# Optimization experiments

Hardware: AMD Instinct MI355X
Metric: run time of the kernel (lower is better)

The kernel has to match this reference:

```python
import jax, jax.numpy as jnp
import numpy as np

HIDDEN = 2048
NUM_HEADS = 32
NUM_GROUPS = 8
HEAD_DIM = HIDDEN // NUM_HEADS          # 64
GROUP_DIM = HEAD_DIM * NUM_GROUPS       # 512
HPG = NUM_HEADS // NUM_GROUPS           # heads per group = 4
B, S = 2, 2048


def setup_inputs() -> dict:
    key = jax.random.key(0)
    ks = jax.random.split(key, 6)
    sd = 1.0 / np.sqrt(HIDDEN)
    return {
        "x": jax.random.normal(ks[0], (B, S, HIDDEN), jnp.float32),
        "mask": jnp.ones((1, 1, S, S), jnp.int32),
        "Wq": jax.random.normal(ks[1], (HIDDEN, HIDDEN), jnp.float32) * sd,
        "bq": jnp.zeros((HIDDEN,), jnp.float32),
        "Wk": jax.random.normal(ks[2], (HIDDEN, GROUP_DIM), jnp.float32) * sd,
        "bk": jnp.zeros((GROUP_DIM,), jnp.float32),
        "Wv": jax.random.normal(ks[3], (HIDDEN, GROUP_DIM), jnp.float32) * sd,
        "bv": jnp.zeros((GROUP_DIM,), jnp.float32),
        "Wo": jax.random.normal(ks[4], (HIDDEN, HIDDEN), jnp.float32) * sd,
        "bo": jnp.zeros((HIDDEN,), jnp.float32),
    }


def reference(x, mask, Wq, bq, Wk, bk, Wv, bv, Wo, bo):
    b, s, _ = x.shape
    # projections
    q = x @ Wq + bq                                        # [B,S,H*d]
    k = x @ Wk + bk                                        # [B,S,G*d]
    v = x @ Wv + bv
    # split heads: q heads are group-major (g, p) to match the torch view
    q = q.reshape(b, s, NUM_GROUPS, HPG, HEAD_DIM)         # [B,S,G,P,d]
    k = k.reshape(b, s, NUM_GROUPS, HEAD_DIM)              # [B,S,G,d]
    v = v.reshape(b, s, NUM_GROUPS, HEAD_DIM)
    scale = 1.0 / np.sqrt(HEAD_DIM).astype(np.float32)
    # grouped attention without materializing repeated K/V
    scores = jnp.einsum('bsgpd,btgd->bgpst', q, k) * scale  # [B,G,P,S,T]
    if mask is not None:
        m = mask[:, :, None]                                # [1,1,1,S,T]
        scores = jnp.where(m == 0, jnp.float32(-1e9), scores)
    weights = jax.nn.softmax(scores, axis=-1)
    out = jnp.einsum('bgpst,btgd->bsgpd', weights, v)       # [B,S,G,P,d]
    out = out.reshape(b, s, HIDDEN)
    return out @ Wo + bo
```

## Files before the change

### kernel.cpp

```cpp
#include <hip/hip_runtime.h>
#include <hip/hip_bf16.h>


#define DEVINL __device__ __forceinline__

typedef __attribute__((ext_vector_type(8))) short bf16x8;
typedef __attribute__((ext_vector_type(4))) float f32x4;

DEVINL unsigned short f2bf(float f) {
  unsigned u = __builtin_bit_cast(unsigned, f);
  u += 0x7fffu + ((u >> 16) & 1u);
  return (unsigned short)(u >> 16);
}

DEVINL unsigned pk2bf(float a, float b) {
  __hip_bfloat162 h = __float22bfloat162_rn(float2{a, b});
  unsigned r;
  __builtin_memcpy(&r, &h, 4);
  return r;
}

DEVINL void gl_lds16(const void* g, void* l) {
  __builtin_amdgcn_global_load_lds(
      (const __attribute__((address_space(1))) void*)g,
      (__attribute__((address_space(3))) void*)l, 16, 0, 0);
}

__global__ __launch_bounds__(256)
void prep_k(const float* __restrict__ x,
            const float* __restrict__ Wq, const float* __restrict__ Wk,
            const float* __restrict__ Wv, const float* __restrict__ Wo,
            const int* __restrict__ mask,
            unsigned short* __restrict__ xb,
            unsigned short* __restrict__ WqT, unsigned short* __restrict__ WkT,
            unsigned short* __restrict__ WvT, unsigned short* __restrict__ WoT,
            int* __restrict__ flags)
{
  __shared__ float tile[64][68];
  __shared__ int fl[4];
  int blk = blockIdx.x;
  const int tid = threadIdx.x;
  if (blk < 4096) {
    size_t base = (size_t)blk * 2048 + tid * 8;
    float4 f0 = *(const float4*)&x[base];
    float4 f1 = *(const float4*)&x[base + 4];
    uint4 o;
    o.x = pk2bf(f0.x, f0.y); o.y = pk2bf(f0.z, f0.w);
    o.z = pk2bf(f1.x, f1.y); o.w = pk2bf(f1.z, f1.w);
    *(uint4*)&xb[base] = o;
    return;
  }
  blk -= 4096;
  if (blk >= 2560) {
    int fb = blk - 2560;
    int qt = fb >> 5, tt = fb & 31;
    bool hz = false;
#pragma unroll
    for (int it = 0; it < 8; ++it) {
      int l = it * 1024 + tid * 4;
      int row = l >> 6, col = l & 63;
      int4 mv = *(const int4*)&mask[(size_t)(qt * 128 + row) * 2048 + tt * 64 + col];
      hz |= (mv.x == 0) | (mv.y == 0) | (mv.z == 0) | (mv.w == 0);
    }
    unsigned long long bal = __ballot(hz);
    if ((tid & 63) == 0) fl[tid >> 6] = (bal != 0ull) ? 1 : 0;
    __syncthreads();
    if (tid == 0) flags[fb] = fl[0] | fl[1] | fl[2] | fl[3];
    return;
  }
  const float* W; unsigned short* WT; int N;
  if (blk < 1024)      { W = Wq; WT = WqT; N = 2048; }
  else if (blk < 1280) { W = Wk; WT = WkT; N = 512;  blk -= 1024; }
  else if (blk < 1536) { W = Wv; WT = WvT; N = 512;  blk -= 1280; }
  else                 { W = Wo; WT = WoT; N = 2048; blk -= 1536; }
  const int kt = blk & 31, nt = blk >> 5;
  const int k0 = kt * 64, n0 = nt * 64;
  const int tr = tid >> 4, tc4 = (tid & 15) * 4;
#pragma unroll
  for (int it = 0; it < 4; ++it) {
    int k = it * 16 + tr;
    float4 v = *(const float4*)&W[(size_t)(k0 + k) * N + n0 + tc4];
    tile[tc4 + 0][k] = v.x; tile[tc4 + 1][k] = v.y;
    tile[tc4 + 2][k] = v.z; tile[tc4 + 3][k] = v.w;
  }
  __syncthreads();
#pragma unroll
  for (int it = 0; it < 4; ++it) {
    int n = it * 16 + tr;
    uint2 o;
    o.x = pk2bf(tile[n][tc4 + 0], tile[n][tc4 + 1]);
    o.y = pk2bf(tile[n][tc4 + 2], tile[n][tc4 + 3]);
    *(uint2*)&WT[(size_t)(n0 + n) * 2048 + k0 + tc4] = o;
  }
}

__global__ __launch_bounds__(256)
void mm_qkv(const unsigned short* __restrict__ A,
            const unsigned short* __restrict__ Wt,
            const float* __restrict__ bq, const float* __restrict__ bk,
            const float* __restrict__ bv,
            unsigned short* __restrict__ qb, unsigned short* __restrict__ kb,
            unsigned short* __restrict__ vb)
{
  __shared__ __align__(16) unsigned short As[128 * 32];
  __shared__ __align__(16) unsigned short Bs[128 * 32];
  const int tid = threadIdx.x;
  const int lane = tid & 63, w = tid >> 6;
  const int l15 = lane & 15, quad = lane >> 4;
  const int wm = w & 1, wn = w >> 1;
  const int row0 = blockIdx.y * 128;
  const int col0 = blockIdx.x * 128;

  f32x4 acc[4][4];
#pragma unroll
  for (int mt = 0; mt < 4; ++mt)
#pragma unroll
    for (int nt = 0; nt < 4; ++nt) acc[mt][nt] = (f32x4){0.f, 0.f, 0.f, 0.f};

  const int c0 = tid, c1 = 256 + tid;
  const size_t aoff0 = (size_t)(row0 + (c0 >> 2)) * 2048 + (c0 & 3) * 8;
  const size_t aoff1 = (size_t)(row0 + (c1 >> 2)) * 2048 + (c1 & 3) * 8;
  const size_t boff0 = (size_t)(col0 + (c0 >> 2)) * 2048 + (c0 & 3) * 8;
  const size_t boff1 = (size_t)(col0 + (c1 >> 2)) * 2048 + (c1 & 3) * 8;

  for (int k0 = 0; k0 < 2048; k0 += 32) {
    gl_lds16(A + aoff0 + k0, As + (size_t)c0 * 8);
    gl_lds16(A + aoff1 + k0, As + (size_t)c1 * 8);
    gl_lds16(Wt + boff0 + k0, Bs + (size_t)c0 * 8);
    gl_lds16(Wt + boff1 + k0, Bs + (size_t)c1 * 8);
    __syncthreads();
    bf16x8 af[4], bfr[4];
#pragma unroll
    for (int mt = 0; mt < 4; ++mt)
      af[mt] = *(const bf16x8*)&As[(wm * 64 + mt * 16 + l15) * 32 + quad * 8];
#pragma unroll
    for (int nt = 0; nt < 4; ++nt)
      bfr[nt] = *(const bf16x8*)&Bs[(wn * 64 + nt * 16 + l15) * 32 + quad * 8];
#pragma unroll
    for (int mt = 0; mt < 4; ++mt)
#pragma unroll
      for (int nt = 0; nt < 4; ++nt)
        acc[mt][nt] = __builtin_amdgcn_mfma_f32_16x16x32_bf16(
            af[mt], bfr[nt], acc[mt][nt], 0, 0, 0);
    __syncthreads();
  }

  const int rbase = row0 + wm * 64 + quad * 4;
#pragma unroll
  for (int nt = 0; nt < 4; ++nt) {
    const int cg = col0 + wn * 64 + nt * 16 + l15;
#pragma unroll
    for (int mt = 0; mt < 4; ++mt) {
#pragma unroll
      for (int reg = 0; reg < 4; ++reg) {
        const int r = rbase + mt * 16 + reg;
        const int bb = r >> 11, ss = r & 2047;
        float v = acc[mt][nt][reg];
        if (col0 < 2048) {
          v += bq[cg];
          int g = cg >> 8, p = (cg >> 6) & 3, d = cg & 63;
          qb[(((size_t)((bb * 8 + g) * 4 + p)) * 2048 + ss) * 64 + d] =
              f2bf(v * 0.1803368801111244f);
        } else if (col0 < 2560) {
          int cl = cg - 2048;
          v += bk[cl];
          int g = cl >> 6, d = cl & 63;
          kb[((size_t)(bb * 8 + g) * 2048 + ss) * 64 + d] = f2bf(v);
        } else {
          int cl = cg - 2560;
          v += bv[cl];
          int g = cl >> 6, d = cl & 63;
          vb[((size_t)(bb * 8 + g) * 64 + d) * 2048 + ss] = f2bf(v);
        }
      }
    }
  }
}

__global__ __launch_bounds__(256)
void mm_out(const unsigned short* __restrict__ A,
            const unsigned short* __restrict__ Bt,
            const float* __restrict__ bias, float* __restrict__ Of)
{
  __shared__ __align__(16) unsigned short As[128 * 32];
  __shared__ __align__(16) unsigned short Bs[128 * 32];
  const int tid = threadIdx.x;
  const int lane = tid & 63, w = tid >> 6;
  const int l15 = lane & 15, quad = lane >> 4;
  const int wm = w & 1, wn = w >> 1;
  const int row0 = blockIdx.y * 128;
  const int col0 = blockIdx.x * 128;

  f32x4 acc[4][4];
#pragma unroll
  for (int mt = 0; mt < 4; ++mt)
#pragma unroll
    for (int nt = 0; nt < 4; ++nt) acc[mt][nt] = (f32x4){0.f, 0.f, 0.f, 0.f};

  const int c0 = tid, c1 = 256 + tid;
  const size_t aoff0 = (size_t)(row0 + (c0 >> 2)) * 2048 + (c0 & 3) * 8;
  const size_t aoff1 = (size_t)(row0 + (c1 >> 2)) * 2048 + (c1 & 3) * 8;
  const size_t boff0 = (size_t)(col0 + (c0 >> 2)) * 2048 + (c0 & 3) * 8;
  const size_t boff1 = (size_t)(col0 + (c1 >> 2)) * 2048 + (c1 & 3) * 8;

  for (int k0 = 0; k0 < 2048; k0 += 32) {
    gl_lds16(A + aoff0 + k0, As + (size_t)c0 * 8);
    gl_lds16(A + aoff1 + k0, As + (size_t)c1 * 8);
    gl_lds16(Bt + boff0 + k0, Bs + (size_t)c0 * 8);
    gl_lds16(Bt + boff1 + k0, Bs + (size_t)c1 * 8);
    __syncthreads();
    bf16x8 af[4], bfr[4];
#pragma unroll
    for (int mt = 0; mt < 4; ++mt)
      af[mt] = *(const bf16x8*)&As[(wm * 64 + mt * 16 + l15) * 32 + quad * 8];
#pragma unroll
    for (int nt = 0; nt < 4; ++nt)
      bfr[nt] = *(const bf16x8*)&Bs[(wn * 64 + nt * 16 + l15) * 32 + quad * 8];
#pragma unroll
    for (int mt = 0; mt < 4; ++mt)
#pragma unroll
      for (int nt = 0; nt < 4; ++nt)
        acc[mt][nt] = __builtin_amdgcn_mfma_f32_16x16x32_bf16(
            af[mt], bfr[nt], acc[mt][nt], 0, 0, 0);
    __syncthreads();
  }

  const int rbase = row0 + wm * 64 + quad * 4;
#pragma unroll
  for (int nt = 0; nt < 4; ++nt) {
    const int cg = col0 + wn * 64 + nt * 16 + l15;
    const float bvv = bias[cg];
#pragma unroll
    for (int mt = 0; mt < 4; ++mt)
#pragma unroll
      for (int reg = 0; reg < 4; ++reg) {
        const int r = rbase + mt * 16 + reg;
        Of[(size_t)r * 2048 + cg] = acc[mt][nt][reg] + bvv;
      }
  }
}

__global__ __launch_bounds__(256, 4)
void attn_k(const unsigned short* __restrict__ qb,
            const unsigned short* __restrict__ kb,
            const unsigned short* __restrict__ vb,
            const int* __restrict__ mask, const int* __restrict__ flags,
            unsigned short* __restrict__ attnb)
{
  __shared__ __align__(16) unsigned short Ks[64 * 64];
  __shared__ __align__(16) unsigned short Vs[64 * 64];
  __shared__ __align__(16) unsigned short Ps[128 * 72];
  const int tid = threadIdx.x;
  const int lane = tid & 63, w = tid >> 6;
  const int l15 = lane & 15, quad = lane >> 4;
  const int q0 = blockIdx.x * 128;
  const int pr = blockIdx.y;
  const int b = pr >> 5, g = (pr >> 2) & 7, p = pr & 3;
  const int bg = b * 8 + g;

  const unsigned short* Kg = kb + (size_t)bg * 2048 * 64;
  const unsigned short* Vg = vb + (size_t)bg * 64 * 2048;
  const unsigned short* Qg = qb + (size_t)(bg * 4 + p) * 2048 * 64;

  bf16x8 qf[2][2];
#pragma unroll
  for (int u = 0; u < 2; ++u) {
    const size_t qrow = (size_t)(q0 + w * 32 + u * 16 + l15) * 64;
    qf[u][0] = *(const bf16x8*)&Qg[qrow + quad * 8];
    qf[u][1] = *(const bf16x8*)&Qg[qrow + 32 + quad * 8];
  }

  bf16x8 ones;
#pragma unroll
  for (int i = 0; i < 8; ++i) ones[i] = (short)0x3F80;

  f32x4 acc_o[4][2];
  f32x4 acc_l[2];
#pragma unroll
  for (int u = 0; u < 2; ++u) acc_l[u] = (f32x4){0.f, 0.f, 0.f, 0.f};
#pragma unroll
  for (int dt = 0; dt < 4; ++dt)
#pragma unroll
    for (int u = 0; u < 2; ++u) acc_o[dt][u] = (f32x4){0.f, 0.f, 0.f, 0.f};

  const int c0 = tid, c1 = 256 + tid;
  const int kr0 = c0 >> 3, kx0 = ((c0 & 7) ^ (kr0 & 7)) * 8;
  const int kr1 = c1 >> 3, kx1 = ((c1 & 7) ^ (kr1 & 7)) * 8;

  for (int t0 = 0; t0 < 2048; t0 += 64) {
    __syncthreads();
    gl_lds16(Kg + (size_t)(t0 + kr0) * 64 + kx0, Ks + (size_t)c0 * 8);
    gl_lds16(Kg + (size_t)(t0 + kr1) * 64 + kx1, Ks + (size_t)c1 * 8);
    gl_lds16(Vg + (size_t)kr0 * 2048 + t0 + kx0, Vs + (size_t)c0 * 8);
    gl_lds16(Vg + (size_t)kr1 * 2048 + t0 + kx1, Vs + (size_t)c1 * 8);
    __syncthreads();

    bf16x8 kf[4][2];
#pragma unroll
    for (int nt = 0; nt < 4; ++nt) {
      const int trow = nt * 16 + l15, ks = trow & 7;
      kf[nt][0] = *(const bf16x8*)&Ks[trow * 64 + ((quad ^ ks) * 8)];
      kf[nt][1] = *(const bf16x8*)&Ks[trow * 64 + (((4 + quad) ^ ks) * 8)];
    }
    const bool msk = flags[blockIdx.x * 32 + (t0 >> 6)] != 0;

#pragma unroll
    for (int u = 0; u < 2; ++u) {
      f32x4 st[4];
#pragma unroll
      for (int nt = 0; nt < 4; ++nt) {
        f32x4 z = (f32x4){0.f, 0.f, 0.f, 0.f};
        z = __builtin_amdgcn_mfma_f32_16x16x32_bf16(kf[nt][0], qf[u][0], z, 0, 0, 0);
        st[nt] = __builtin_amdgcn_mfma_f32_16x16x32_bf16(kf[nt][1], qf[u][1], z, 0, 0, 0);
      }
      if (msk) {
        const size_t mrow = (size_t)(q0 + w * 32 + u * 16 + l15) * 2048;
#pragma unroll
        for (int nt = 0; nt < 4; ++nt) {
          int4 mv = *(const int4*)&mask[mrow + t0 + nt * 16 + quad * 4];
          if (mv.x == 0) st[nt][0] = -1e30f;
          if (mv.y == 0) st[nt][1] = -1e30f;
          if (mv.z == 0) st[nt][2] = -1e30f;
          if (mv.w == 0) st[nt][3] = -1e30f;
        }
      }
      const int srow = w * 32 + u * 16 + l15;
#pragma unroll
      for (int nt = 0; nt < 4; ++nt) {
        float p0 = __builtin_amdgcn_exp2f(st[nt][0]);
        float p1 = __builtin_amdgcn_exp2f(st[nt][1]);
        float p2 = __builtin_amdgcn_exp2f(st[nt][2]);
        float p3 = __builtin_amdgcn_exp2f(st[nt][3]);
        uint2 pkd;
        pkd.x = pk2bf(p0, p1);
        pkd.y = pk2bf(p2, p3);
        *(uint2*)&Ps[srow * 72 + nt * 16 + quad * 4] = pkd;
      }
    }
    asm volatile("s_waitcnt lgkmcnt(0)" ::: "memory");

    bf16x8 pf[2][2];
#pragma unroll
    for (int u = 0; u < 2; ++u) {
      const int srow = w * 32 + u * 16 + l15;
      pf[u][0] = *(const bf16x8*)&Ps[srow * 72 + quad * 8];
      pf[u][1] = *(const bf16x8*)&Ps[srow * 72 + 32 + quad * 8];
      acc_l[u] = __builtin_amdgcn_mfma_f32_16x16x32_bf16(ones, pf[u][0], acc_l[u], 0, 0, 0);
      acc_l[u] = __builtin_amdgcn_mfma_f32_16x16x32_bf16(ones, pf[u][1], acc_l[u], 0, 0, 0);
    }
#pragma unroll
    for (int dt = 0; dt < 4; ++dt) {
      const int drow = dt * 16 + l15, ks = drow & 7;
      bf16x8 v0 = *(const bf16x8*)&Vs[drow * 64 + ((quad ^ ks) * 8)];
      bf16x8 v1 = *(const bf16x8*)&Vs[drow * 64 + (((4 + quad) ^ ks) * 8)];
#pragma unroll
      for (int u = 0; u < 2; ++u) {
        acc_o[dt][u] = __builtin_amdgcn_mfma_f32_16x16x32_bf16(v0, pf[u][0], acc_o[dt][u], 0, 0, 0);
        acc_o[dt][u] = __builtin_amdgcn_mfma_f32_16x16x32_bf16(v1, pf[u][1], acc_o[dt][u], 0, 0, 0);
      }
    }
  }

  const int hh = g * 4 + p;
#pragma unroll
  for (int u = 0; u < 2; ++u) {
    const float inv = 1.0f / acc_l[u][0];
    const int s = q0 + w * 32 + u * 16 + l15;
#pragma unroll
    for (int dt = 0; dt < 4; ++dt) {
      uint2 o;
      o.x = pk2bf(acc_o[dt][u][0] * inv, acc_o[dt][u][1] * inv);
      o.y = pk2bf(acc_o[dt][u][2] * inv, acc_o[dt][u][3] * inv);
      *(uint2*)&attnb[((size_t)(b * 2048 + s)) * 2048 + hh * 64 + dt * 16 + quad * 4] = o;
    }
  }
}

extern "C" void kernel_launch(void* const* d_in, const int* in_sizes, int n_in,
                              void* d_out, int out_size, void* d_ws, size_t ws_size,
                              hipStream_t stream)
{
  (void)in_sizes; (void)n_in; (void)out_size; (void)ws_size;
  const float* x  = (const float*)d_in[0];
  const int* mask = (const int*)d_in[1];
  const float* Wq = (const float*)d_in[2];
  const float* bq = (const float*)d_in[3];
  const float* Wk = (const float*)d_in[4];
  const float* bk = (const float*)d_in[5];
  const float* Wv = (const float*)d_in[6];
  const float* bv = (const float*)d_in[7];
  const float* Wo = (const float*)d_in[8];
  const float* bo = (const float*)d_in[9];
  float* out = (float*)d_out;

  unsigned short* xb  = (unsigned short*)d_ws;
  unsigned short* WqT = xb  + 8388608;
  unsigned short* WkT = WqT + 4194304;
  unsigned short* WvT = WkT + 1048576;
  unsigned short* WoT = WvT + 1048576;
  unsigned short* qb  = WoT + 4194304;
  unsigned short* kb  = qb  + 8388608;
  unsigned short* vb  = kb  + 2097152;
  int* flags = (int*)(vb + 2097152);
  unsigned short* attnb = xb;

  dim3 blk(256);
  hipLaunchKernelGGL(prep_k, dim3(7168), blk, 0, stream,
                     x, Wq, Wk, Wv, Wo, mask, xb, WqT, WkT, WvT, WoT, flags);
  hipLaunchKernelGGL(mm_qkv, dim3(24, 32), blk, 0, stream,
                     xb, WqT, bq, bk, bv, qb, kb, vb);
  hipLaunchKernelGGL(attn_k, dim3(16, 64), blk, 0, stream,
                     qb, kb, vb, mask, flags, attnb);
  hipLaunchKernelGGL(mm_out, dim3(16, 32), blk, 0, stream,
                     attnb, WoT, bo, out);
}
```

Before: 361.7 us.

## Double-buffer K/V tiles in attention kernel to overlap loads with compute

The attention kernel gets two shared-memory buffers each for K and V. The next 64-key tile is fetched with direct global-to-LDS loads while the current tile is processed, and each iteration now ends with a single barrier instead of two. The aim is to hide global-load latency behind the MFMA and softmax work. The cost is more LDS per block, so launch bounds drop from 4 to 3 blocks per CU, which lowers occupancy.

```diff
diff --git a/kernel.cpp b/kernel.cpp
--- a/kernel.cpp
+++ b/kernel.cpp
@@ -240,15 +240,15 @@
   }
 }
 
-__global__ __launch_bounds__(256, 4)
+__global__ __launch_bounds__(256, 3)
 void attn_k(const unsigned short* __restrict__ qb,
             const unsigned short* __restrict__ kb,
             const unsigned short* __restrict__ vb,
             const int* __restrict__ mask, const int* __restrict__ flags,
             unsigned short* __restrict__ attnb)
 {
-  __shared__ __align__(16) unsigned short Ks[64 * 64];
-  __shared__ __align__(16) unsigned short Vs[64 * 64];
+  __shared__ __align__(16) unsigned short Ks[2][64 * 64];
+  __shared__ __align__(16) unsigned short Vs[2][64 * 64];
   __shared__ __align__(16) unsigned short Ps[128 * 72];
   const int tid = threadIdx.x;
   const int lane = tid & 63, w = tid >> 6;
@@ -287,22 +287,33 @@
   const int kr0 = c0 >> 3, kx0 = ((c0 & 7) ^ (kr0 & 7)) * 8;
   const int kr1 = c1 >> 3, kx1 = ((c1 & 7) ^ (kr1 & 7)) * 8;
 
-  for (int t0 = 0; t0 < 2048; t0 += 64) {
-    __syncthreads();
-    gl_lds16(Kg + (size_t)(t0 + kr0) * 64 + kx0, Ks + (size_t)c0 * 8);
-    gl_lds16(Kg + (size_t)(t0 + kr1) * 64 + kx1, Ks + (size_t)c1 * 8);
-    gl_lds16(Vg + (size_t)kr0 * 2048 + t0 + kx0, Vs + (size_t)c0 * 8);
-    gl_lds16(Vg + (size_t)kr1 * 2048 + t0 + kx1, Vs + (size_t)c1 * 8);
-    __syncthreads();
+  gl_lds16(Kg + (size_t)kr0 * 64 + kx0, &Ks[0][(size_t)c0 * 8]);
+  gl_lds16(Kg + (size_t)kr1 * 64 + kx1, &Ks[0][(size_t)c1 * 8]);
+  gl_lds16(Vg + (size_t)kr0 * 2048 + kx0, &Vs[0][(size_t)c0 * 8]);
+  gl_lds16(Vg + (size_t)kr1 * 2048 + kx1, &Vs[0][(size_t)c1 * 8]);
+  __syncthreads();
+
+  for (int it = 0; it < 32; ++it) {
+    const int cur = it & 1;
+    const int t0 = it << 6;
+    if (it < 31) {
+      const int tn = t0 + 64;
+      gl_lds16(Kg + (size_t)(tn + kr0) * 64 + kx0, &Ks[cur ^ 1][(size_t)c0 * 8]);
+      gl_lds16(Kg + (size_t)(tn + kr1) * 64 + kx1, &Ks[cur ^ 1][(size_t)c1 * 8]);
+      gl_lds16(Vg + (size_t)kr0 * 2048 + tn + kx0, &Vs[cur ^ 1][(size_t)c0 * 8]);
+      gl_lds16(Vg + (size_t)kr1 * 2048 + tn + kx1, &Vs[cur ^ 1][(size_t)c1 * 8]);
+    }
+    const unsigned short* Kc = Ks[cur];
+    const unsigned short* Vc = Vs[cur];
 
     bf16x8 kf[4][2];
 #pragma unroll
     for (int nt = 0; nt < 4; ++nt) {
       const int trow = nt * 16 + l15, ks = trow & 7;
-      kf[nt][0] = *(const bf16x8*)&Ks[trow * 64 + ((quad ^ ks) * 8)];
-      kf[nt][1] = *(const bf16x8*)&Ks[trow * 64 + (((4 + quad) ^ ks) * 8)];
-    }
-    const bool msk = flags[blockIdx.x * 32 + (t0 >> 6)] != 0;
+      kf[nt][0] = *(const bf16x8*)&Kc[trow * 64 + ((quad ^ ks) * 8)];
+      kf[nt][1] = *(const bf16x8*)&Kc[trow * 64 + (((4 + quad) ^ ks) * 8)];
+    }
+    const bool msk = flags[blockIdx.x * 32 + it] != 0;
 
 #pragma unroll
     for (int u = 0; u < 2; ++u) {
@@ -351,14 +362,15 @@
 #pragma unroll
     for (int dt = 0; dt < 4; ++dt) {
       const int drow = dt * 16 + l15, ks = drow & 7;
-      bf16x8 v0 = *(const bf16x8*)&Vs[drow * 64 + ((quad ^ ks) * 8)];
-      bf16x8 v1 = *(const bf16x8*)&Vs[drow * 64 + (((4 + quad) ^ ks) * 8)];
+      bf16x8 v0 = *(const bf16x8*)&Vc[drow * 64 + ((quad ^ ks) * 8)];
+      bf16x8 v1 = *(const bf16x8*)&Vc[drow * 64 + (((4 + quad) ^ ks) * 8)];
 #pragma unroll
       for (int u = 0; u < 2; ++u) {
         acc_o[dt][u] = __builtin_amdgcn_mfma_f32_16x16x32_bf16(v0, pf[u][0], acc_o[dt][u], 0, 0, 0);
         acc_o[dt][u] = __builtin_amdgcn_mfma_f32_16x16x32_bf16(v1, pf[u][1], acc_o[dt][u], 0, 0, 0);
       }
     }
+    __syncthreads();
   }
 
   const int hh = g * 4 + p;
```

Result: faster. 348.8 us (-3.6%).
